# Kernel tuning notes

Measured on AMD Instinct MI355X. Metric: run time of the kernel, lower is better.

## Reference

```python
import jax, jax.numpy as jnp
import numpy as np

TEMPERATURE = 1.0

def setup_inputs() -> dict:
    key = jax.random.key(0)
    k1, k2 = jax.random.split(key)
    z1 = jax.random.normal(k1, (8, 256, 2048), dtype=jnp.float32)
    z2 = jax.random.normal(k2, (8, 256, 2048), dtype=jnp.float32)
    return {"z1": z1, "z2": z2}

def reference(z1, z2):
    # logits[b, n, m] = sum_s z1[b, s, n] * z2[b, s, m], scaled by temperature
    logits = jnp.einsum('bsn,bsm->bnm', z1, z2) / TEMPERATURE
    # torch F.cross_entropy on (b, C=n, m) with labels[b, m] = m:
    # softmax over axis 1 (n), then gather the diagonal n == m.
    logp = jax.nn.log_softmax(logits, axis=1)        # (b, n, m)
    diag = jnp.diagonal(logp, axis1=1, axis2=2)      # (b, m) = logp[b, m, m]
    return -jnp.mean(diag)
```

## Files before the change

kernel.cpp:

```cpp
#include <hip/hip_runtime.h>
#include <hip/hip_bf16.h>


#define NN 2048
#define SK 256
#define LDST 264
#define LOG2E 1.4426950408889634f
#define LN2   0.6931471805599453f
#define COFF  96.0f

typedef __attribute__((ext_vector_type(8))) short short8;
typedef __attribute__((ext_vector_type(16))) float f32x16;

__device__ __forceinline__ unsigned short f2bf(float f) {
    __hip_bfloat16 h = __float2bfloat16(f);
    unsigned short u; __builtin_memcpy(&u, &h, 2); return u;
}

__device__ __forceinline__ float exp2g(float x) {
#if __has_builtin(__builtin_amdgcn_exp2f)
    return __builtin_amdgcn_exp2f(x);
#else
    return exp2f(x);
#endif
}

__device__ __forceinline__ float log2g(float x) {
#if __has_builtin(__builtin_amdgcn_logf)
    return __builtin_amdgcn_logf(x);
#else
    return log2f(x);
#endif
}

__global__ __launch_bounds__(512) void gemm_lse_kernel(
    const float* __restrict__ z1, const float* __restrict__ z2,
    float* __restrict__ ws_sum, float* __restrict__ ws_diag)
{
    __shared__ unsigned short lds[256 * LDST];

    const int bid  = blockIdx.x;
    const int b    = bid & 7;
    const int tile = bid >> 3;
    const int mb   = tile & 3;
    const int ns   = tile >> 2;
    const int tid  = threadIdx.x;
    const int lane = tid & 63;
    const int w    = tid >> 6;
    const int col  = lane & 31;
    const int kg   = lane >> 5;

    const int m0      = mb * 512 + w * 64;
    const int mcol0   = m0 + col;
    const int mcol1   = m0 + 32 + col;
    const int n_start = ns * 256;

    const float* z1b = z1 + (size_t)b * SK * NN;
    const float* z2b = z2 + (size_t)b * SK * NN;

    const int kc  = (w << 1) | kg;
    const int row = col;
    #pragma unroll
    for (int rg = 0; rg < 8; ++rg) {
        const int nrow = rg * 32 + row;
        const float* p = z1b + (size_t)(kc * 16) * NN + (n_start + nrow);
        float t0[8], t1[8];
        #pragma unroll
        for (int j = 0; j < 8; ++j) t0[j] = p[(size_t)j * NN];
        #pragma unroll
        for (int j = 0; j < 8; ++j) t1[j] = p[(size_t)(j + 8) * NN];
        short8 pk0, pk1;
        #pragma unroll
        for (int j = 0; j < 8; ++j) { pk0[j] = (short)f2bf(t0[j]); pk1[j] = (short)f2bf(t1[j]); }
        *(short8*)(lds + nrow * LDST + kc * 16)     = pk0;
        *(short8*)(lds + nrow * LDST + kc * 16 + 8) = pk1;
    }

    short8 bf0[16], bf1[16];
    #pragma unroll
    for (int ks = 0; ks < 16; ++ks) {
        short8 p0, p1;
        #pragma unroll
        for (int j = 0; j < 8; ++j) {
            const int s = ks * 16 + kg * 8 + j;
            p0[j] = (short)f2bf(z2b[(size_t)s * NN + mcol0] * LOG2E);
            p1[j] = (short)f2bf(z2b[(size_t)s * NN + mcol1] * LOG2E);
        }
        bf0[ks] = p0; bf1[ks] = p1;
    }

    float srun0 = 0.0f, srun1 = 0.0f;

    __syncthreads();

    #pragma unroll 2
    for (int sub = 0; sub < 8; ++sub) {
        const unsigned short* abase = lds + (32 * sub + col) * LDST + kg * 8;

        f32x16 acc0, acc1;
        #pragma unroll
        for (int r = 0; r < 16; ++r) { acc0[r] = -COFF; acc1[r] = -COFF; }

        #pragma unroll
        for (int ks = 0; ks < 16; ++ks) {
            short8 af = *(const short8*)(abase + ks * 16);
            acc0 = __builtin_amdgcn_mfma_f32_32x32x16_bf16(af, bf0[ks], acc0, 0, 0, 0);
            acc1 = __builtin_amdgcn_mfma_f32_32x32x16_bf16(af, bf1[ks], acc1, 0, 0, 0);
        }

        const int nsub = n_start + 32 * sub;
        if (nsub == m0) {
            #pragma unroll
            for (int r = 0; r < 16; ++r) {
                const int rw = (r & 3) + 8 * (r >> 2) + 4 * kg;
                if (rw == col) ws_diag[b * NN + mcol0] = acc0[r];
            }
        }
        if (nsub == m0 + 32) {
            #pragma unroll
            for (int r = 0; r < 16; ++r) {
                const int rw = (r & 3) + 8 * (r >> 2) + 4 * kg;
                if (rw == col) ws_diag[b * NN + mcol1] = acc1[r];
            }
        }

        {
            float e0 = 0, e1 = 0, e2 = 0, e3 = 0;
            #pragma unroll
            for (int r = 0; r < 16; r += 4) {
                e0 += exp2g(acc0[r]);     e1 += exp2g(acc0[r + 1]);
                e2 += exp2g(acc0[r + 2]); e3 += exp2g(acc0[r + 3]);
            }
            srun0 += (e0 + e1) + (e2 + e3);
        }
        {
            float e0 = 0, e1 = 0, e2 = 0, e3 = 0;
            #pragma unroll
            for (int r = 0; r < 16; r += 4) {
                e0 += exp2g(acc1[r]);     e1 += exp2g(acc1[r + 1]);
                e2 += exp2g(acc1[r + 2]); e3 += exp2g(acc1[r + 3]);
            }
            srun1 += (e0 + e1) + (e2 + e3);
        }
    }

    srun0 += __shfl_xor(srun0, 32);
    srun1 += __shfl_xor(srun1, 32);
    if (kg == 0) {
        ws_sum[(b * 8 + ns) * NN + mcol0] = srun0;
        ws_sum[(b * 8 + ns) * NN + mcol1] = srun1;
    }
}

__global__ __launch_bounds__(256) void merge_kernel(
    const float* __restrict__ ws_sum, const float* __restrict__ ws_diag,
    float* __restrict__ partial)
{
    const int gid = blockIdx.x * 256 + threadIdx.x;
    const int b = gid >> 11, m = gid & (NN - 1);

    float S = 0.0f;
    #pragma unroll
    for (int slot = 0; slot < 8; ++slot)
        S += ws_sum[(b * 8 + slot) * NN + m];
    float c = log2g(S) - ws_diag[gid];

    #pragma unroll
    for (int d = 1; d < 64; d <<= 1) c += __shfl_xor(c, d);
    __shared__ float red[4];
    if ((threadIdx.x & 63) == 0) red[threadIdx.x >> 6] = c;
    __syncthreads();
    if (threadIdx.x == 0)
        partial[blockIdx.x] = red[0] + red[1] + red[2] + red[3];
}

__global__ void final_kernel(const float* __restrict__ partial, float* __restrict__ out)
{
    float v = partial[threadIdx.x];
    #pragma unroll
    for (int d = 1; d < 64; d <<= 1) v += __shfl_xor(v, d);
    if (threadIdx.x == 0) out[0] = v * (LN2 / 16384.0f);
}

extern "C" void kernel_launch(void* const* d_in, const int* in_sizes, int n_in,
                              void* d_out, int out_size, void* d_ws, size_t ws_size,
                              hipStream_t stream)
{
    const float* z1 = (const float*)d_in[0];
    const float* z2 = (const float*)d_in[1];
    float* ws  = (float*)d_ws;
    float* out = (float*)d_out;

    float* ws_sum  = ws;
    float* ws_diag = ws + 131072;
    float* ws_part = ws + 147456;

    gemm_lse_kernel<<<dim3(256), dim3(512), 0, stream>>>(z1, z2, ws_sum, ws_diag);
    merge_kernel<<<dim3(64), dim3(256), 0, stream>>>(ws_sum, ws_diag, ws_part);
    final_kernel<<<dim3(1), dim3(64), 0, stream>>>(ws_part, out);
}
```

Before: 29.15 us.

## Fuse merge and final reductions into GEMM kernel via last-block atomic counters

Removes the separate merge and final kernel launches. Each GEMM block bumps an atomic counter for its (batch, m-block) group, and the last of the 8 arriving blocks does that group's log-sum and diagonal merge. A second counter picks the last group, which writes the final mean. This saves two kernel launch gaps at the cost of a memset node, thread fences and atomics in the tail of the GEMM kernel.

After: 70.81 us. 143% more time.

```diff
diff --git a/kernel.cpp b/kernel.cpp
--- a/kernel.cpp
+++ b/kernel.cpp
@@ -35,9 +35,13 @@
 
 __global__ __launch_bounds__(512) void gemm_lse_kernel(
     const float* __restrict__ z1, const float* __restrict__ z2,
-    float* __restrict__ ws_sum, float* __restrict__ ws_diag)
+    float* __restrict__ ws_sum, float* __restrict__ ws_diag,
+    float* __restrict__ partial, unsigned int* __restrict__ ctr,
+    float* __restrict__ out)
 {
     __shared__ unsigned short lds[256 * LDST];
+    __shared__ float red[8];
+    __shared__ int amLastI;
 
     const int bid  = blockIdx.x;
     const int b    = bid & 7;
@@ -150,36 +154,50 @@
         ws_sum[(b * 8 + ns) * NN + mcol0] = srun0;
         ws_sum[(b * 8 + ns) * NN + mcol1] = srun1;
     }
-}
-
-__global__ __launch_bounds__(256) void merge_kernel(
-    const float* __restrict__ ws_sum, const float* __restrict__ ws_diag,
-    float* __restrict__ partial)
-{
-    const int gid = blockIdx.x * 256 + threadIdx.x;
-    const int b = gid >> 11, m = gid & (NN - 1);
-
-    float S = 0.0f;
-    #pragma unroll
-    for (int slot = 0; slot < 8; ++slot)
-        S += ws_sum[(b * 8 + slot) * NN + m];
-    float c = log2g(S) - ws_diag[gid];
-
-    #pragma unroll
-    for (int d = 1; d < 64; d <<= 1) c += __shfl_xor(c, d);
-    __shared__ float red[4];
-    if ((threadIdx.x & 63) == 0) red[threadIdx.x >> 6] = c;
+
+    const int cidx = b * 4 + mb;
+
+    __threadfence();
     __syncthreads();
-    if (threadIdx.x == 0)
-        partial[blockIdx.x] = red[0] + red[1] + red[2] + red[3];
-}
-
-__global__ void final_kernel(const float* __restrict__ partial, float* __restrict__ out)
-{
-    float v = partial[threadIdx.x];
-    #pragma unroll
-    for (int d = 1; d < 64; d <<= 1) v += __shfl_xor(v, d);
-    if (threadIdx.x == 0) out[0] = v * (LN2 / 16384.0f);
+    if (tid == 0) {
+        unsigned int old = atomicAdd(&ctr[cidx], 1u);
+        amLastI = (old == 7u);
+    }
+    __syncthreads();
+
+    if (amLastI) {
+        __threadfence();
+        volatile const float* vsum  = ws_sum;
+        volatile const float* vdiag = ws_diag;
+
+        const int m = mb * 512 + tid;
+        float S = 0.0f;
+        #pragma unroll
+        for (int slot = 0; slot < 8; ++slot)
+            S += vsum[(b * 8 + slot) * NN + m];
+        float c = log2g(S) - vdiag[b * NN + m];
+
+        #pragma unroll
+        for (int d = 1; d < 64; d <<= 1) c += __shfl_xor(c, d);
+        if ((tid & 63) == 0) red[tid >> 6] = c;
+        __syncthreads();
+
+        if (tid == 0) {
+            float s = 0.0f;
+            #pragma unroll
+            for (int i = 0; i < 8; ++i) s += red[i];
+            partial[cidx] = s;
+            __threadfence();
+            unsigned int old2 = atomicAdd(&ctr[32], 1u);
+            if (old2 == 31u) {
+                __threadfence();
+                volatile const float* vp = partial;
+                float tot = 0.0f;
+                for (int i = 0; i < 32; ++i) tot += vp[i];
+                out[0] = tot * (LN2 / 16384.0f);
+            }
+        }
+    }
 }
 
 extern "C" void kernel_launch(void* const* d_in, const int* in_sizes, int n_in,
@@ -194,8 +212,10 @@
     float* ws_sum  = ws;
     float* ws_diag = ws + 131072;
     float* ws_part = ws + 147456;
-
-    gemm_lse_kernel<<<dim3(256), dim3(512), 0, stream>>>(z1, z2, ws_sum, ws_diag);
-    merge_kernel<<<dim3(64), dim3(256), 0, stream>>>(ws_sum, ws_diag, ws_part);
-    final_kernel<<<dim3(1), dim3(64), 0, stream>>>(ws_part, out);
-}
+    unsigned int* ws_ctr = (unsigned int*)(ws + 147488);
+
+    hipMemsetAsync((void*)ws_ctr, 0, 256, stream);
+
+    gemm_lse_kernel<<<dim3(256), dim3(512), 0, stream>>>(
+        z1, z2, ws_sum, ws_diag, ws_part, ws_ctr, out);
+}
```
